# Optimization experiments

Measured on AMD Instinct MI355X. Metric: run time of the kernel, lower is better.

The kernel has to match this reference:

```python
import jax, jax.numpy as jnp
import numpy as np

N_NODES = 50000
N_EDGES = 3200000
FEAT_IN = 2048  # pools 2:1 down to 1024


def _gcn_conv(x, row, col, W, b, n):
    # PyG GCNConv: add self-loops, symmetric D^-1/2 (A+I) D^-1/2 normalization,
    # aggregate at target (col), then bias.
    xw = x @ W  # [n, out]
    ones = jnp.ones(row.shape[0], dtype=xw.dtype)
    deg = jax.ops.segment_sum(ones, col, num_segments=n)  # includes self-loops
    dis = jax.lax.rsqrt(deg)  # deg >= 1 because of self-loops
    norm = dis[row] * dis[col]  # [E+n]
    out = jax.ops.segment_sum(norm[:, None] * xw[row], col, num_segments=n)
    return out + b


def setup_inputs() -> dict:
    key = jax.random.key(0)
    ks = jax.random.split(key, 12)
    x = jax.random.normal(ks[0], (N_NODES, FEAT_IN), dtype=jnp.float32)
    edge_index = jax.random.randint(ks[1], (2, N_EDGES), 0, N_NODES, dtype=jnp.int64)
    def lin(k, fan_in, fan_out):
        s = 1.0 / np.sqrt(fan_in)
        kw, kb = jax.random.split(k)
        W = jax.random.uniform(kw, (fan_in, fan_out), jnp.float32, -s, s)
        b = jax.random.uniform(kb, (fan_out,), jnp.float32, -s, s)
        return W, b
    w0, b0 = lin(ks[2], 1024, 512)
    w1, b1 = lin(ks[3], 512, 128)
    w2, b2 = lin(ks[4], 128, 64)
    g1_w, g1_b = lin(ks[5], 64, 32)
    g2_w, g2_b = lin(ks[6], 32, 16)
    return {
        "x": x, "edge_index": edge_index,
        "ln_w": jnp.ones((1024,), jnp.float32), "ln_b": jnp.zeros((1024,), jnp.float32),
        "w0": w0, "b0": b0, "w1": w1, "b1": b1, "w2": w2, "b2": b2,
        "g1_w": g1_w, "g1_b": g1_b, "g2_w": g2_w, "g2_b": g2_b,
    }


def reference(x, edge_index, ln_w, ln_b, w0, b0, w1, b1, w2, b2, g1_w, g1_b, g2_w, g2_b):
    n = x.shape[0]
    # AdaptiveMaxPool1d(1024): L=2048 -> exact windows of 2, stride 2
    h = x.reshape(n, 1024, 2).max(axis=-1)
    # LayerNorm(1024)
    mu = h.mean(axis=-1, keepdims=True)
    var = jnp.mean((h - mu) ** 2, axis=-1, keepdims=True)
    h = (h - mu) * jax.lax.rsqrt(var + 1e-5) * ln_w + ln_b
    # MLP with ELU (dropout is identity in eval mode)
    h = jax.nn.elu(h @ w0 + b0)
    h = jax.nn.elu(h @ w1 + b1)
    h = jax.nn.elu(h @ w2 + b2)
    # edge_index with self-loops appended (constant structure)
    sl = jnp.arange(n, dtype=edge_index.dtype)
    row = jnp.concatenate([edge_index[0], sl])
    col = jnp.concatenate([edge_index[1], sl])
    h = jax.nn.elu(_gcn_conv(h, row, col, g1_w, g1_b, n))
    return _gcn_conv(h, row, col, g2_w, g2_b, n)
```

## Files before the change

kernel.cpp:

```cpp
#include <hip/hip_runtime.h>
#include <hip/hip_bf16.h>

#define N_NODES 50000
#define N_EDGES 3200000
#define NB1 196
#define NBLK1 782
#define CAP 20480

typedef __bf16 v8bf __attribute__((ext_vector_type(8)));
typedef __bf16 v2bf __attribute__((ext_vector_type(2)));
typedef float v4f __attribute__((ext_vector_type(4)));

__device__ __forceinline__ float elu_f(float x) { return x > 0.f ? x : (expf(x) - 1.f); }

#define GL16(gp, lp) __builtin_amdgcn_global_load_lds( \
    (const __attribute__((address_space(1))) void*)(gp), \
    (__attribute__((address_space(3))) void*)(lp), 16, 0, 0)

__global__ void pool_ln_kernel(const float* __restrict__ x,
                               const float* __restrict__ ln_w,
                               const float* __restrict__ ln_b,
                               __bf16* __restrict__ h0) {
    int wave = threadIdx.x >> 6, lane = threadIdx.x & 63;
    int node = blockIdx.x * 4 + wave;
    const float4* xr = (const float4*)(x + (size_t)node * 2048);
    float4 v[8];
    #pragma unroll
    for (int j = 0; j < 8; ++j) v[j] = xr[j * 64 + lane];
    float p[16];
    float sum = 0.f, sq = 0.f;
    #pragma unroll
    for (int j = 0; j < 8; ++j) {
        p[2 * j]     = fmaxf(v[j].x, v[j].y);
        p[2 * j + 1] = fmaxf(v[j].z, v[j].w);
        sum += p[2 * j] + p[2 * j + 1];
        sq  += p[2 * j] * p[2 * j] + p[2 * j + 1] * p[2 * j + 1];
    }
    #pragma unroll
    for (int off = 32; off > 0; off >>= 1) {
        sum += __shfl_xor(sum, off);
        sq  += __shfl_xor(sq, off);
    }
    float mu = sum * (1.f / 1024.f);
    float var = sq * (1.f / 1024.f) - mu * mu;
    float rstd = rsqrtf(var + 1e-5f);
    const float2* w2p = (const float2*)ln_w;
    const float2* b2p = (const float2*)ln_b;
    #pragma unroll
    for (int j = 0; j < 8; ++j) {
        int c2 = j * 64 + lane;
        float2 w = w2p[c2], b = b2p[c2];
        v2bf o;
        o[0] = (__bf16)((p[2 * j]     - mu) * rstd * w.x + b.x);
        o[1] = (__bf16)((p[2 * j + 1] - mu) * rstd * w.y + b.y);
        *(v2bf*)(h0 + (size_t)node * 1024 + 2 * c2) = o;
    }
}

__global__ void wt_all_kernel(const float* __restrict__ w0, const float* __restrict__ w1,
                              const float* __restrict__ w2,
                              __bf16* __restrict__ w0t, __bf16* __restrict__ w1t,
                              __bf16* __restrict__ w2t, int* __restrict__ fill196) {
    int idx = blockIdx.x * 256 + threadIdx.x;
    if (idx < NB1) fill196[idx] = idx * CAP;
    if (idx < 524288) {
        int k = idx >> 9, n = idx & 511;
        w0t[(size_t)n * 1024 + k] = (__bf16)w0[idx];
    } else if (idx < 524288 + 65536) {
        int j = idx - 524288;
        int k = j >> 7, n = j & 127;
        w1t[(size_t)n * 512 + k] = (__bf16)w1[j];
    } else if (idx < 524288 + 65536 + 8192) {
        int j = idx - 524288 - 65536;
        int k = j >> 6, n = j & 63;
        w2t[(size_t)n * 128 + k] = (__bf16)w2[j];
    }
}

__global__ __launch_bounds__(512) void mfma_gemm0(
    const __bf16* __restrict__ A, const __bf16* __restrict__ BT,
    const float* __restrict__ bias, __bf16* __restrict__ C, int M)
{
    const int K = 1024, N = 512;
    __shared__ unsigned short lds[12288];
    const int tid = threadIdx.x;
    const int lane = tid & 63, w = tid >> 6;
    const int wr = w >> 2, wc = w & 3;
    const int m0 = blockIdx.x * 128, n0 = blockIdx.y * 256;

    int grA = m0 + (tid >> 2); if (grA > M - 1) grA = M - 1;
    const __bf16* aP = A + (size_t)grA * K + (tid & 3) * 8;
    char* ldsA = (char*)lds + tid * 16;
    const __bf16* bP0 = BT + (size_t)(n0 + (tid >> 2)) * K + (tid & 3) * 8;
    const __bf16* bP1 = BT + (size_t)(n0 + ((tid + 512) >> 2)) * K + (tid & 3) * 8;
    char* ldsB0 = (char*)lds + 8192 + tid * 16;
    char* ldsB1 = (char*)lds + 16384 + tid * 16;

    v4f acc[4][4] = {};
    const int l15 = lane & 15, l4 = lane >> 4;
    const int abase = (wr * 64 + l15) * 32 + l4 * 8;
    const int bbase = 4096 + (wc * 64 + l15) * 32 + l4 * 8;

    for (int k0 = 0; k0 < K; k0 += 32) {
        GL16(aP + k0, ldsA);
        GL16(bP0 + k0, ldsB0);
        GL16(bP1 + k0, ldsB1);
        __syncthreads();
        v8bf af[4], bfr[4];
        #pragma unroll
        for (int m = 0; m < 4; ++m) af[m]  = *(const v8bf*)&lds[abase + m * 16 * 32];
        #pragma unroll
        for (int n = 0; n < 4; ++n) bfr[n] = *(const v8bf*)&lds[bbase + n * 16 * 32];
        #pragma unroll
        for (int m = 0; m < 4; ++m)
            #pragma unroll
            for (int n = 0; n < 4; ++n)
                acc[m][n] = __builtin_amdgcn_mfma_f32_16x16x32_bf16(af[m], bfr[n], acc[m][n], 0, 0, 0);
        __syncthreads();
    }

    #pragma unroll
    for (int m = 0; m < 4; ++m) {
        #pragma unroll
        for (int j = 0; j < 4; ++j) {
            int row = m0 + wr * 64 + m * 16 + l4 * 4 + j;
            if (row >= M) continue;
            #pragma unroll
            for (int n = 0; n < 4; ++n) {
                int col = n0 + wc * 64 + n * 16 + l15;
                float v = acc[m][n][j] + bias[col];
                C[(size_t)row * N + col] = (__bf16)elu_f(v);
            }
        }
    }
}

__global__ __launch_bounds__(256) void mlp_tail_kernel(
    const __bf16* __restrict__ h1, const __bf16* __restrict__ w1t,
    const float* __restrict__ b1, const __bf16* __restrict__ w2t,
    const float* __restrict__ b2, const float* __restrict__ g1w,
    const float* __restrict__ dis, float* __restrict__ xw1, int M)
{
    extern __shared__ char smem[];
    const int G1OFF = 32768, TOFF = 40960;
    const int tid = threadIdx.x;
    const int lane = tid & 63, wave = tid >> 6;
    const int l15 = lane & 15, l4 = lane >> 4;
    const int m0 = blockIdx.x * 128;

    {
        const float4* g4 = (const float4*)g1w;
        float4* d4 = (float4*)(smem + G1OFF);
        d4[tid] = g4[tid];
        d4[tid + 256] = g4[tid + 256];
    }

    const int wr = wave >> 1, wc = wave & 1;
    const int s0 = tid, s1 = tid + 256;
    int gr0 = m0 + (s0 >> 2); if (gr0 > M - 1) gr0 = M - 1;
    int gr1 = m0 + (s1 >> 2); if (gr1 > M - 1) gr1 = M - 1;
    const __bf16* a0p = h1 + (size_t)gr0 * 512 + (s0 & 3) * 8;
    const __bf16* a1p = h1 + (size_t)gr1 * 512 + (s1 & 3) * 8;
    const __bf16* b0p = w1t + (size_t)(s0 >> 2) * 512 + (s0 & 3) * 8;
    const __bf16* b1p = w1t + (size_t)(s1 >> 2) * 512 + (s1 & 3) * 8;
    char* stA0 = smem + s0 * 16;
    char* stA1 = smem + s1 * 16;
    char* stB0 = smem + 8192 + s0 * 16;
    char* stB1 = smem + 8192 + s1 * 16;
    const int aoff = (wr * 64 + l15) * 64 + l4 * 16;
    const int boff = 8192 + (wc * 64 + l15) * 64 + l4 * 16;

    v4f acc1[4][4] = {};
    for (int k0 = 0; k0 < 512; k0 += 32) {
        GL16(a0p + k0, stA0);
        GL16(a1p + k0, stA1);
        GL16(b0p + k0, stB0);
        GL16(b1p + k0, stB1);
        __syncthreads();
        v8bf af[4], bfr[4];
        #pragma unroll
        for (int m = 0; m < 4; ++m) af[m]  = *(const v8bf*)(smem + aoff + m * 1024);
        #pragma unroll
        for (int n = 0; n < 4; ++n) bfr[n] = *(const v8bf*)(smem + boff + n * 1024);
        #pragma unroll
        for (int m = 0; m < 4; ++m)
            #pragma unroll
            for (int n = 0; n < 4; ++n)
                acc1[m][n] = __builtin_amdgcn_mfma_f32_16x16x32_bf16(af[m], bfr[n], acc1[m][n], 0, 0, 0);
        __syncthreads();
    }
    float b1c[4];
    #pragma unroll
    for (int n = 0; n < 4; ++n) b1c[n] = b1[wc * 64 + n * 16 + l15];
    #pragma unroll
    for (int m = 0; m < 4; ++m) {
        #pragma unroll
        for (int j = 0; j < 4; ++j) {
            int row = wr * 64 + m * 16 + l4 * 4 + j;
            int rx = (row & 7) << 4;
            #pragma unroll
            for (int n = 0; n < 4; ++n) {
                int colb = (wc * 64 + n * 16 + l15) * 2;
                float v = elu_f(acc1[m][n][j] + b1c[n]);
                *(__bf16*)(smem + TOFF + row * 256 + (colb ^ rx)) = (__bf16)v;
            }
        }
    }
    __syncthreads();

    const int wr2 = wave >> 1, wc2 = wave & 1;
    v4f acc2[4][2] = {};
    #pragma unroll
    for (int ks = 0; ks < 4; ++ks) {
        v8bf af2[4], bf2[2];
        #pragma unroll
        for (int m2 = 0; m2 < 4; ++m2) {
            int row = wr2 * 64 + m2 * 16 + l15;
            af2[m2] = *(const v8bf*)(smem + TOFF + row * 256 + ((ks * 64 + l4 * 16) ^ ((row & 7) << 4)));
        }
        #pragma unroll
        for (int n2 = 0; n2 < 2; ++n2) {
            int nn = wc2 * 32 + n2 * 16 + l15;
            bf2[n2] = *(const v8bf*)(w2t + nn * 128 + ks * 32 + l4 * 8);
        }
        #pragma unroll
        for (int m2 = 0; m2 < 4; ++m2)
            #pragma unroll
            for (int n2 = 0; n2 < 2; ++n2)
                acc2[m2][n2] = __builtin_amdgcn_mfma_f32_16x16x32_bf16(af2[m2], bf2[n2], acc2[m2][n2], 0, 0, 0);
    }
    __syncthreads();
    float b2c[2];
    #pragma unroll
    for (int n2 = 0; n2 < 2; ++n2) b2c[n2] = b2[wc2 * 32 + n2 * 16 + l15];
    #pragma unroll
    for (int m2 = 0; m2 < 4; ++m2) {
        #pragma unroll
        for (int j = 0; j < 4; ++j) {
            int row = wr2 * 64 + m2 * 16 + l4 * 4 + j;
            int rx = (row & 7) << 4;
            #pragma unroll
            for (int n2 = 0; n2 < 2; ++n2) {
                int col = wc2 * 32 + n2 * 16 + l15;
                float v = elu_f(acc2[m2][n2][j] + b2c[n2]);
                *(float*)(smem + row * 256 + ((col * 4) ^ rx)) = v;
            }
        }
    }
    __syncthreads();

    int r = tid >> 1;
    int nb = (tid & 1) * 16;
    int gr = m0 + r;
    float o[16] = {};
    int rx = (r & 7) << 4;
    #pragma unroll 4
    for (int k4 = 0; k4 < 16; ++k4) {
        float4 h4 = *(const float4*)(smem + r * 256 + ((k4 * 16) ^ rx));
        #pragma unroll
        for (int e = 0; e < 4; ++e) {
            const float4* gp = (const float4*)(smem + G1OFF + (k4 * 4 + e) * 128 + nb * 4);
            float hv = (e == 0) ? h4.x : (e == 1) ? h4.y : (e == 2) ? h4.z : h4.w;
            #pragma unroll
            for (int q = 0; q < 4; ++q) {
                float4 g = gp[q];
                o[4 * q + 0] += hv * g.x;
                o[4 * q + 1] += hv * g.y;
                o[4 * q + 2] += hv * g.z;
                o[4 * q + 3] += hv * g.w;
            }
        }
    }
    if (gr < M) {
        float d = dis[gr];
        #pragma unroll
        for (int q = 0; q < 4; ++q) {
            float4 v;
            v.x = o[4 * q + 0] * d; v.y = o[4 * q + 1] * d;
            v.z = o[4 * q + 2] * d; v.w = o[4 * q + 3] * d;
            *(float4*)(xw1 + (size_t)gr * 32 + nb + 4 * q) = v;
        }
    }
}

__global__ void gemm_kernel(const float* __restrict__ A, const float* __restrict__ W,
                            const float* __restrict__ bias, const float* __restrict__ scale,
                            float* __restrict__ C, int M, int N, int K, int do_elu) {
    const int BM = 64, BN = 64, BK = 16;
    __shared__ float As[BK][BM + 4];
    __shared__ float Ws[BK][BN + 4];
    int tid = threadIdx.x;
    int tx = tid & 15, ty = tid >> 4;
    int m0 = blockIdx.x * BM;
    int n0 = blockIdx.y * BN;
    float acc[4][4] = {};
    for (int k0 = 0; k0 < K; k0 += BK) {
        #pragma unroll
        for (int l = 0; l < 4; ++l) {
            int idx = tid + l * 256;
            int r = idx >> 4, c = idx & 15;
            int m = m0 + r;
            As[c][r] = (m < M) ? A[(size_t)m * K + k0 + c] : 0.f;
        }
        #pragma unroll
        for (int l = 0; l < 4; ++l) {
            int idx = tid + l * 256;
            int c = idx >> 6, n = idx & 63;
            int nn = n0 + n;
            Ws[c][n] = (nn < N) ? W[(size_t)(k0 + c) * N + nn] : 0.f;
        }
        __syncthreads();
        #pragma unroll
        for (int kk = 0; kk < BK; ++kk) {
            float4 av = *(const float4*)&As[kk][ty * 4];
            float4 wv = *(const float4*)&Ws[kk][tx * 4];
            float ar[4] = {av.x, av.y, av.z, av.w};
            float wrg[4] = {wv.x, wv.y, wv.z, wv.w};
            #pragma unroll
            for (int i = 0; i < 4; ++i)
                #pragma unroll
                for (int j = 0; j < 4; ++j)
                    acc[i][j] += ar[i] * wrg[j];
        }
        __syncthreads();
    }
    #pragma unroll
    for (int i = 0; i < 4; ++i) {
        int m = m0 + ty * 4 + i;
        if (m >= M) continue;
        float sc = scale ? scale[m] : 1.f;
        #pragma unroll
        for (int j = 0; j < 4; ++j) {
            int n = n0 + tx * 4 + j;
            if (n >= N) continue;
            float v = acc[i][j] + (bias ? bias[n] : 0.f);
            if (do_elu) v = elu_f(v);
            C[(size_t)m * N + n] = v * sc;
        }
    }
}

__global__ void p1_scatter_kernel(const int* __restrict__ row, const int* __restrict__ col,
                                  int* __restrict__ fill196, unsigned int* __restrict__ tmp) {
    __shared__ int h[NB1], bl[NB1];
    int t = threadIdx.x, b = blockIdx.x;
    if (t < NB1) h[t] = 0;
    __syncthreads();
    int base = b * 4096;
    int cc[16];
    #pragma unroll
    for (int j = 0; j < 16; ++j) {
        int e = base + j * 256 + t;
        cc[j] = (e < N_EDGES) ? col[e] : -1;
        if (cc[j] >= 0) atomicAdd(&h[cc[j] >> 8], 1);
    }
    __syncthreads();
    if (t < NB1 && h[t] > 0) bl[t] = atomicAdd(&fill196[t], h[t]);
    __syncthreads();
    #pragma unroll
    for (int j = 0; j < 16; ++j) {
        if (cc[j] >= 0) {
            int e = base + j * 256 + t;
            int pos = atomicAdd(&bl[cc[j] >> 8], 1);
            tmp[pos] = ((unsigned int)cc[j] << 16) | (unsigned int)row[e];
        }
    }
}
__global__ void p2_kernel(const unsigned int* __restrict__ tmp, const int* __restrict__ fill196,
                          int* __restrict__ csr, int* __restrict__ ptr, float* __restrict__ dis) {
    __shared__ int h2[256], b2[256], s2[256];
    __shared__ int sh_outb;
    int seg = blockIdx.x;
    int start = seg * CAP, end = fill196[seg];
    int t = threadIdx.x;
    if (t < 256) s2[t] = (t < seg) ? (fill196[t] - t * CAP) : 0;
    __syncthreads();
    for (int off = 128; off > 0; off >>= 1) {
        if (t < off) s2[t] += s2[t + off];
        __syncthreads();
    }
    if (t == 0) sh_outb = s2[0];
    if (t < 256) h2[t] = 0;
    __syncthreads();
    for (int i = start + t; i < end; i += 1024)
        atomicAdd(&h2[(tmp[i] >> 16) & 255], 1);
    __syncthreads();
    if (t < 256) s2[t] = h2[t];
    __syncthreads();
    for (int off = 1; off < 256; off <<= 1) {
        int u = 0;
        if (t < 256 && t >= off) u = s2[t - off];
        __syncthreads();
        if (t < 256) s2[t] += u;
        __syncthreads();
    }
    if (t < 256) {
        int p = sh_outb + s2[t] - h2[t];
        b2[t] = p;
        int node = (seg << 8) + t;
        if (node < N_NODES) {
            ptr[node] = p;
            dis[node] = rsqrtf((float)(h2[t] + 1));
        }
    }
    if (seg == NB1 - 1 && t == 0) ptr[N_NODES] = N_EDGES;
    __syncthreads();
    for (int i = start + t; i < end; i += 1024) {
        unsigned int v = tmp[i];
        int pos = atomicAdd(&b2[(v >> 16) & 255], 1);
        csr[pos] = (int)(v & 0xFFFFu);
    }
}

__global__ void gather_kernel(const float* __restrict__ xws, const int* __restrict__ csr,
                              const int* __restrict__ ptr, const float* __restrict__ dis,
                              const float* __restrict__ bias, float* __restrict__ out,
                              int f4shift, int do_elu) {
    int idx = blockIdx.x * 256 + threadIdx.x;
    int node = idx >> f4shift;
    if (node >= N_NODES) return;
    int q = idx & ((1 << f4shift) - 1);
    int s = ptr[node], e = ptr[node + 1];
    const float4* xw4 = (const float4*)xws;
    float4 acc = xw4[((size_t)node << f4shift) + q];
    int i = s;
    for (; i + 4 <= e; i += 4) {
        int r0 = csr[i], r1 = csr[i + 1], r2 = csr[i + 2], r3 = csr[i + 3];
        float4 va = xw4[((size_t)r0 << f4shift) + q];
        float4 vb = xw4[((size_t)r1 << f4shift) + q];
        float4 vc = xw4[((size_t)r2 << f4shift) + q];
        float4 vd = xw4[((size_t)r3 << f4shift) + q];
        acc.x += (va.x + vb.x) + (vc.x + vd.x);
        acc.y += (va.y + vb.y) + (vc.y + vd.y);
        acc.z += (va.z + vb.z) + (vc.z + vd.z);
        acc.w += (va.w + vb.w) + (vc.w + vd.w);
    }
    for (; i < e; ++i) {
        int r = csr[i];
        float4 v = xw4[((size_t)r << f4shift) + q];
        acc.x += v.x; acc.y += v.y; acc.z += v.z; acc.w += v.w;
    }
    float d = dis[node];
    float4 bb = ((const float4*)bias)[q];
    float4 o;
    o.x = d * acc.x + bb.x; o.y = d * acc.y + bb.y;
    o.z = d * acc.z + bb.z; o.w = d * acc.w + bb.w;
    if (do_elu) { o.x = elu_f(o.x); o.y = elu_f(o.y); o.z = elu_f(o.z); o.w = elu_f(o.w); }
    ((float4*)out)[idx] = o;
}

extern "C" void kernel_launch(void* const* d_in, const int* in_sizes, int n_in,
                              void* d_out, int out_size, void* d_ws, size_t ws_size,
                              hipStream_t stream) {
    const float* x    = (const float*)d_in[0];
    const int*   ei   = (const int*)d_in[1];
    const int*   row  = ei;
    const int*   col  = ei + N_EDGES;
    const float* ln_w = (const float*)d_in[2];
    const float* ln_b = (const float*)d_in[3];
    const float* w0   = (const float*)d_in[4];
    const float* b0   = (const float*)d_in[5];
    const float* w1   = (const float*)d_in[6];
    const float* b1   = (const float*)d_in[7];
    const float* w2   = (const float*)d_in[8];
    const float* b2   = (const float*)d_in[9];
    const float* g1w  = (const float*)d_in[10];
    const float* g1b  = (const float*)d_in[11];
    const float* g2w  = (const float*)d_in[12];
    const float* g2b  = (const float*)d_in[13];
    float* out = (float*)d_out;

    char* W = (char*)d_ws;
    __bf16* h0  = (__bf16*)(W + 0);
    __bf16* h1  = (__bf16*)(W + 102400000);
    float*  dis = (float*) (W + 179200000);
    float*  xw1 = (float*) (W + 179400192);
    float*  agg1= (float*) (W + 185800192);
    float*  xw2 = (float*) (W + 192200192);
    __bf16* w0t = (__bf16*)(W + 195400192);
    __bf16* w1t = (__bf16*)(W + 196448768);
    __bf16* w2t = (__bf16*)(W + 196579840);
    int*    csr  = (int*)(W + 200000000);
    int*    ptr  = (int*)(W + 213000192);
    unsigned int* tmp = (unsigned int*)(W + 214000128);
    int*    fill196 = (int*)(W + 231000064);

    wt_all_kernel<<<(598016 + 255) / 256, 256, 0, stream>>>(w0, w1, w2, w0t, w1t, w2t, fill196);

    pool_ln_kernel<<<N_NODES / 4, 256, 0, stream>>>(x, ln_w, ln_b, h0);

    {
        dim3 g((N_NODES + 127) / 128, 2);
        mfma_gemm0<<<g, 512, 0, stream>>>(h0, w0t, b0, h1, N_NODES);
    }

    p1_scatter_kernel<<<NBLK1, 256, 0, stream>>>(row, col, fill196, tmp);
    p2_kernel<<<NB1, 1024, 0, stream>>>(tmp, fill196, csr, ptr, dis);

    mlp_tail_kernel<<<(N_NODES + 127) / 128, 256, 73728, stream>>>(
        h1, w1t, b1, w2t, b2, g1w, dis, xw1, N_NODES);

    gather_kernel<<<((N_NODES * 8) + 255) / 256, 256, 0, stream>>>(
        xw1, csr, ptr, dis, g1b, agg1, 3, 1);

    {
        dim3 g((N_NODES + 63) / 64, 1);
        gemm_kernel<<<g, 256, 0, stream>>>(agg1, g2w, nullptr, dis, xw2, N_NODES, 16, 32, 0);
    }
    gather_kernel<<<((N_NODES * 4) + 255) / 256, 256, 0, stream>>>(
        xw2, csr, ptr, dis, g2b, out, 2, 0);
}
```

Measured before the change: 405.8 us.

## Fuse GCN layer-2 linear into first gather and store gathered features in bf16

Folds the weight-transpose kernel into the pool/LayerNorm launch. Fuses the second GCN linear (32->16) into the first aggregation kernel using LDS-resident weights and a cross-lane shuffle reduction. Stores the per-node transformed features xw1/xw2 as bf16 to halve the random gather traffic. This removes two launches and an fp32 intermediate round trip, at the cost of reduced precision in the aggregated features and extra shuffle work per node.

```diff
diff --git a/kernel.cpp b/kernel.cpp
--- a/kernel.cpp
+++ b/kernel.cpp
@@ -13,6 +13,15 @@
 
 __device__ __forceinline__ float elu_f(float x) { return x > 0.f ? x : (expf(x) - 1.f); }
 
+__device__ __forceinline__ float4 bf4f(ushort4 u) {
+    float4 r;
+    r.x = __uint_as_float(((unsigned)u.x) << 16);
+    r.y = __uint_as_float(((unsigned)u.y) << 16);
+    r.z = __uint_as_float(((unsigned)u.z) << 16);
+    r.w = __uint_as_float(((unsigned)u.w) << 16);
+    return r;
+}
+
 #define GL16(gp, lp) __builtin_amdgcn_global_load_lds( \
     (const __attribute__((address_space(1))) void*)(gp), \
     (__attribute__((address_space(3))) void*)(lp), 16, 0, 0)
@@ -20,8 +29,29 @@
 __global__ void pool_ln_kernel(const float* __restrict__ x,
                                const float* __restrict__ ln_w,
                                const float* __restrict__ ln_b,
-                               __bf16* __restrict__ h0) {
-    int wave = threadIdx.x >> 6, lane = threadIdx.x & 63;
+                               __bf16* __restrict__ h0,
+                               const float* __restrict__ w0, const float* __restrict__ w1,
+                               const float* __restrict__ w2,
+                               __bf16* __restrict__ w0t, __bf16* __restrict__ w1t,
+                               __bf16* __restrict__ w2t, int* __restrict__ fill196) {
+    int t = threadIdx.x;
+    if (blockIdx.x < 2336) {
+        int idx = blockIdx.x * 256 + t;
+        if (idx < NB1) fill196[idx] = idx * CAP;
+        if (idx < 524288) {
+            int k = idx >> 9, n = idx & 511;
+            w0t[(size_t)n * 1024 + k] = (__bf16)w0[idx];
+        } else if (idx < 524288 + 65536) {
+            int j = idx - 524288;
+            int k = j >> 7, n = j & 127;
+            w1t[(size_t)n * 512 + k] = (__bf16)w1[j];
+        } else if (idx < 524288 + 65536 + 8192) {
+            int j = idx - 524288 - 65536;
+            int k = j >> 6, n = j & 63;
+            w2t[(size_t)n * 128 + k] = (__bf16)w2[j];
+        }
+    }
+    int wave = t >> 6, lane = t & 63;
     int node = blockIdx.x * 4 + wave;
     const float4* xr = (const float4*)(x + (size_t)node * 2048);
     float4 v[8];
@@ -54,26 +84,6 @@
         o[0] = (__bf16)((p[2 * j]     - mu) * rstd * w.x + b.x);
         o[1] = (__bf16)((p[2 * j + 1] - mu) * rstd * w.y + b.y);
         *(v2bf*)(h0 + (size_t)node * 1024 + 2 * c2) = o;
-    }
-}
-
-__global__ void wt_all_kernel(const float* __restrict__ w0, const float* __restrict__ w1,
-                              const float* __restrict__ w2,
-                              __bf16* __restrict__ w0t, __bf16* __restrict__ w1t,
-                              __bf16* __restrict__ w2t, int* __restrict__ fill196) {
-    int idx = blockIdx.x * 256 + threadIdx.x;
-    if (idx < NB1) fill196[idx] = idx * CAP;
-    if (idx < 524288) {
-        int k = idx >> 9, n = idx & 511;
-        w0t[(size_t)n * 1024 + k] = (__bf16)w0[idx];
-    } else if (idx < 524288 + 65536) {
-        int j = idx - 524288;
-        int k = j >> 7, n = j & 127;
-        w1t[(size_t)n * 512 + k] = (__bf16)w1[j];
-    } else if (idx < 524288 + 65536 + 8192) {
-        int j = idx - 524288 - 65536;
-        int k = j >> 6, n = j & 63;
-        w2t[(size_t)n * 128 + k] = (__bf16)w2[j];
     }
 }
 
@@ -139,7 +149,7 @@
     const __bf16* __restrict__ h1, const __bf16* __restrict__ w1t,
     const float* __restrict__ b1, const __bf16* __restrict__ w2t,
     const float* __restrict__ b2, const float* __restrict__ g1w,
-    const float* __restrict__ dis, float* __restrict__ xw1, int M)
+    const float* __restrict__ dis, __bf16* __restrict__ xw1b, int M)
 {
     extern __shared__ char smem[];
     const int G1OFF = 32768, TOFF = 40960;
@@ -273,70 +283,14 @@
     }
     if (gr < M) {
         float d = dis[gr];
-        #pragma unroll
-        for (int q = 0; q < 4; ++q) {
-            float4 v;
-            v.x = o[4 * q + 0] * d; v.y = o[4 * q + 1] * d;
-            v.z = o[4 * q + 2] * d; v.w = o[4 * q + 3] * d;
-            *(float4*)(xw1 + (size_t)gr * 32 + nb + 4 * q) = v;
-        }
-    }
-}
-
-__global__ void gemm_kernel(const float* __restrict__ A, const float* __restrict__ W,
-                            const float* __restrict__ bias, const float* __restrict__ scale,
-                            float* __restrict__ C, int M, int N, int K, int do_elu) {
-    const int BM = 64, BN = 64, BK = 16;
-    __shared__ float As[BK][BM + 4];
-    __shared__ float Ws[BK][BN + 4];
-    int tid = threadIdx.x;
-    int tx = tid & 15, ty = tid >> 4;
-    int m0 = blockIdx.x * BM;
-    int n0 = blockIdx.y * BN;
-    float acc[4][4] = {};
-    for (int k0 = 0; k0 < K; k0 += BK) {
-        #pragma unroll
-        for (int l = 0; l < 4; ++l) {
-            int idx = tid + l * 256;
-            int r = idx >> 4, c = idx & 15;
-            int m = m0 + r;
-            As[c][r] = (m < M) ? A[(size_t)m * K + k0 + c] : 0.f;
-        }
-        #pragma unroll
-        for (int l = 0; l < 4; ++l) {
-            int idx = tid + l * 256;
-            int c = idx >> 6, n = idx & 63;
-            int nn = n0 + n;
-            Ws[c][n] = (nn < N) ? W[(size_t)(k0 + c) * N + nn] : 0.f;
-        }
-        __syncthreads();
-        #pragma unroll
-        for (int kk = 0; kk < BK; ++kk) {
-            float4 av = *(const float4*)&As[kk][ty * 4];
-            float4 wv = *(const float4*)&Ws[kk][tx * 4];
-            float ar[4] = {av.x, av.y, av.z, av.w};
-            float wrg[4] = {wv.x, wv.y, wv.z, wv.w};
-            #pragma unroll
-            for (int i = 0; i < 4; ++i)
-                #pragma unroll
-                for (int j = 0; j < 4; ++j)
-                    acc[i][j] += ar[i] * wrg[j];
-        }
-        __syncthreads();
-    }
-    #pragma unroll
-    for (int i = 0; i < 4; ++i) {
-        int m = m0 + ty * 4 + i;
-        if (m >= M) continue;
-        float sc = scale ? scale[m] : 1.f;
-        #pragma unroll
-        for (int j = 0; j < 4; ++j) {
-            int n = n0 + tx * 4 + j;
-            if (n >= N) continue;
-            float v = acc[i][j] + (bias ? bias[n] : 0.f);
-            if (do_elu) v = elu_f(v);
-            C[(size_t)m * N + n] = v * sc;
-        }
+        v8bf pk0, pk1;
+        #pragma unroll
+        for (int j2 = 0; j2 < 8; ++j2) {
+            pk0[j2] = (__bf16)(o[j2] * d);
+            pk1[j2] = (__bf16)(o[8 + j2] * d);
+        }
+        *(v8bf*)(xw1b + (size_t)gr * 32 + nb) = pk0;
+        *(v8bf*)(xw1b + (size_t)gr * 32 + nb + 8) = pk1;
     }
 }
 
@@ -412,40 +366,95 @@
     }
 }
 
-__global__ void gather_kernel(const float* __restrict__ xws, const int* __restrict__ csr,
-                              const int* __restrict__ ptr, const float* __restrict__ dis,
-                              const float* __restrict__ bias, float* __restrict__ out,
-                              int f4shift, int do_elu) {
-    int idx = blockIdx.x * 256 + threadIdx.x;
-    int node = idx >> f4shift;
+__global__ void gather1_kernel(const unsigned short* __restrict__ xw1b,
+                               const int* __restrict__ csr, const int* __restrict__ ptr,
+                               const float* __restrict__ dis, const float* __restrict__ g1b,
+                               const float* __restrict__ g2w, __bf16* __restrict__ xw2b) {
+    __shared__ float g2t[512];
+    int t = threadIdx.x;
+    {
+        int k = t >> 4, n = t & 15;
+        g2t[n * 32 + k] = g2w[t];
+        int j = t + 256;
+        k = j >> 4; n = j & 15;
+        g2t[n * 32 + k] = g2w[j];
+    }
+    __syncthreads();
+    int idx = blockIdx.x * 256 + t;
+    int node = idx >> 3, q = idx & 7;
     if (node >= N_NODES) return;
-    int q = idx & ((1 << f4shift) - 1);
     int s = ptr[node], e = ptr[node + 1];
-    const float4* xw4 = (const float4*)xws;
-    float4 acc = xw4[((size_t)node << f4shift) + q];
+    const ushort4* base = (const ushort4*)xw1b;
+    float4 acc = bf4f(base[(size_t)node * 8 + q]);
     int i = s;
     for (; i + 4 <= e; i += 4) {
-        int r0 = csr[i], r1 = csr[i + 1], r2 = csr[i + 2], r3 = csr[i + 3];
-        float4 va = xw4[((size_t)r0 << f4shift) + q];
-        float4 vb = xw4[((size_t)r1 << f4shift) + q];
-        float4 vc = xw4[((size_t)r2 << f4shift) + q];
-        float4 vd = xw4[((size_t)r3 << f4shift) + q];
-        acc.x += (va.x + vb.x) + (vc.x + vd.x);
-        acc.y += (va.y + vb.y) + (vc.y + vd.y);
-        acc.z += (va.z + vb.z) + (vc.z + vd.z);
-        acc.w += (va.w + vb.w) + (vc.w + vd.w);
+        float4 a = bf4f(base[(size_t)csr[i] * 8 + q]);
+        float4 b = bf4f(base[(size_t)csr[i + 1] * 8 + q]);
+        float4 c = bf4f(base[(size_t)csr[i + 2] * 8 + q]);
+        float4 d4 = bf4f(base[(size_t)csr[i + 3] * 8 + q]);
+        acc.x += (a.x + b.x) + (c.x + d4.x);
+        acc.y += (a.y + b.y) + (c.y + d4.y);
+        acc.z += (a.z + b.z) + (c.z + d4.z);
+        acc.w += (a.w + b.w) + (c.w + d4.w);
     }
     for (; i < e; ++i) {
-        int r = csr[i];
-        float4 v = xw4[((size_t)r << f4shift) + q];
+        float4 v = bf4f(base[(size_t)csr[i] * 8 + q]);
         acc.x += v.x; acc.y += v.y; acc.z += v.z; acc.w += v.w;
     }
     float d = dis[node];
-    float4 bb = ((const float4*)bias)[q];
+    float4 bb = ((const float4*)g1b)[q];
+    float a0 = elu_f(d * acc.x + bb.x);
+    float a1 = elu_f(d * acc.y + bb.y);
+    float a2 = elu_f(d * acc.z + bb.z);
+    float a3 = elu_f(d * acc.w + bb.w);
+    float p[16];
+    const int k0 = 4 * q;
+    #pragma unroll
+    for (int n = 0; n < 16; ++n) {
+        const float* g = &g2t[n * 32 + k0];
+        p[n] = a0 * g[0] + a1 * g[1] + a2 * g[2] + a3 * g[3];
+    }
+    #pragma unroll
+    for (int off = 1; off < 8; off <<= 1)
+        #pragma unroll
+        for (int n = 0; n < 16; ++n)
+            p[n] += __shfl_xor(p[n], off);
+    v2bf o2;
+    o2[0] = (__bf16)(d * p[2 * q]);
+    o2[1] = (__bf16)(d * p[2 * q + 1]);
+    *(v2bf*)(xw2b + (size_t)node * 16 + 2 * q) = o2;
+}
+
+__global__ void gather2_kernel(const unsigned short* __restrict__ xw2b,
+                               const int* __restrict__ csr, const int* __restrict__ ptr,
+                               const float* __restrict__ dis, const float* __restrict__ g2b,
+                               float* __restrict__ out) {
+    int idx = blockIdx.x * 256 + threadIdx.x;
+    int node = idx >> 2, q = idx & 3;
+    if (node >= N_NODES) return;
+    int s = ptr[node], e = ptr[node + 1];
+    const ushort4* base = (const ushort4*)xw2b;
+    float4 acc = bf4f(base[(size_t)node * 4 + q]);
+    int i = s;
+    for (; i + 4 <= e; i += 4) {
+        float4 a = bf4f(base[(size_t)csr[i] * 4 + q]);
+        float4 b = bf4f(base[(size_t)csr[i + 1] * 4 + q]);
+        float4 c = bf4f(base[(size_t)csr[i + 2] * 4 + q]);
+        float4 d4 = bf4f(base[(size_t)csr[i + 3] * 4 + q]);
+        acc.x += (a.x + b.x) + (c.x + d4.x);
+        acc.y += (a.y + b.y) + (c.y + d4.y);
+        acc.z += (a.z + b.z) + (c.z + d4.z);
+        acc.w += (a.w + b.w) + (c.w + d4.w);
+    }
+    for (; i < e; ++i) {
+        float4 v = bf4f(base[(size_t)csr[i] * 4 + q]);
+        acc.x += v.x; acc.y += v.y; acc.z += v.z; acc.w += v.w;
+    }
+    float d = dis[node];
+    float4 bb = ((const float4*)g2b)[q];
     float4 o;
     o.x = d * acc.x + bb.x; o.y = d * acc.y + bb.y;
     o.z = d * acc.z + bb.z; o.w = d * acc.w + bb.w;
-    if (do_elu) { o.x = elu_f(o.x); o.y = elu_f(o.y); o.z = elu_f(o.z); o.w = elu_f(o.w); }
     ((float4*)out)[idx] = o;
 }
 
@@ -471,23 +480,21 @@
     float* out = (float*)d_out;
 
     char* W = (char*)d_ws;
-    __bf16* h0  = (__bf16*)(W + 0);
-    __bf16* h1  = (__bf16*)(W + 102400000);
-    float*  dis = (float*) (W + 179200000);
-    float*  xw1 = (float*) (W + 179400192);
-    float*  agg1= (float*) (W + 185800192);
-    float*  xw2 = (float*) (W + 192200192);
-    __bf16* w0t = (__bf16*)(W + 195400192);
-    __bf16* w1t = (__bf16*)(W + 196448768);
-    __bf16* w2t = (__bf16*)(W + 196579840);
+    __bf16* h0   = (__bf16*)(W + 0);
+    __bf16* h1   = (__bf16*)(W + 102400000);
+    float*  dis  = (float*) (W + 179200000);
+    __bf16* xw1b = (__bf16*)(W + 179400192);
+    __bf16* xw2b = (__bf16*)(W + 185800192);
+    __bf16* w0t  = (__bf16*)(W + 195400192);
+    __bf16* w1t  = (__bf16*)(W + 196448768);
+    __bf16* w2t  = (__bf16*)(W + 196579840);
     int*    csr  = (int*)(W + 200000000);
     int*    ptr  = (int*)(W + 213000192);
     unsigned int* tmp = (unsigned int*)(W + 214000128);
     int*    fill196 = (int*)(W + 231000064);
 
-    wt_all_kernel<<<(598016 + 255) / 256, 256, 0, stream>>>(w0, w1, w2, w0t, w1t, w2t, fill196);
-
-    pool_ln_kernel<<<N_NODES / 4, 256, 0, stream>>>(x, ln_w, ln_b, h0);
+    pool_ln_kernel<<<N_NODES / 4, 256, 0, stream>>>(
+        x, ln_w, ln_b, h0, w0, w1, w2, w0t, w1t, w2t, fill196);
 
     {
         dim3 g((N_NODES + 127) / 128, 2);
@@ -498,15 +505,11 @@
     p2_kernel<<<NB1, 1024, 0, stream>>>(tmp, fill196, csr, ptr, dis);
 
     mlp_tail_kernel<<<(N_NODES + 127) / 128, 256, 73728, stream>>>(
-        h1, w1t, b1, w2t, b2, g1w, dis, xw1, N_NODES);
-
-    gather_kernel<<<((N_NODES * 8) + 255) / 256, 256, 0, stream>>>(
-        xw1, csr, ptr, dis, g1b, agg1, 3, 1);
-
-    {
-        dim3 g((N_NODES + 63) / 64, 1);
-        gemm_kernel<<<g, 256, 0, stream>>>(agg1, g2w, nullptr, dis, xw2, N_NODES, 16, 32, 0);
-    }
-    gather_kernel<<<((N_NODES * 4) + 255) / 256, 256, 0, stream>>>(
-        xw2, csr, ptr, dis, g2b, out, 2, 0);
-}
+        h1, w1t, b1, w2t, b2, g1w, dis, xw1b, N_NODES);
+
+    gather1_kernel<<<((N_NODES * 8) + 255) / 256, 256, 0, stream>>>(
+        (const unsigned short*)xw1b, csr, ptr, dis, g1b, g2w, xw2b);
+
+    gather2_kernel<<<((N_NODES * 4) + 255) / 256, 256, 0, stream>>>(
+        (const unsigned short*)xw2b, csr, ptr, dis, g2b, out);
+}
```

Measured after the change: 376.7 us. 1.08x faster.
